# Kernel tuning notes

Hardware: AMD Instinct MI355X
Metric: run time of the kernel (lower is better)

## Reference

```python
import jax, jax.numpy as jnp
import numpy as np

B = 16384
IN = 512
H = 512

def setup_inputs() -> dict:
    key = jax.random.key(0)
    ks = jax.random.split(key, 8)
    inp = {
        "x_t": jax.random.normal(ks[0], (B, IN), dtype=jnp.float32),
        "h_t": jax.random.normal(ks[1], (B, H), dtype=jnp.float32),
        "W_ir": jax.random.normal(ks[2], (IN, H), dtype=jnp.float32),
        "W_hr": jax.random.normal(ks[3], (H, H), dtype=jnp.float32),
        "b_r": jnp.zeros((H,), dtype=jnp.float32),
        "W_iz": jax.random.normal(ks[4], (IN, H), dtype=jnp.float32),
        "W_hz": jax.random.normal(ks[5], (H, H), dtype=jnp.float32),
        "b_z": jnp.zeros((H,), dtype=jnp.float32),
        "W_in": jax.random.normal(ks[6], (IN, H), dtype=jnp.float32),
        "W_hn": jax.random.normal(ks[7], (H, H), dtype=jnp.float32),
        "b_n": jnp.zeros((H,), dtype=jnp.float32),
    }
    return inp

def reference(x_t, h_t, W_ir, W_hr, b_r, W_iz, W_hz, b_z, W_in, W_hn, b_n):
    # Fuse the three input-side and three hidden-side GEMMs by concatenating weights.
    Wi = jnp.concatenate([W_ir, W_iz, W_in], axis=1)   # [IN, 3H]
    Wh = jnp.concatenate([W_hr, W_hz, W_hn], axis=1)   # [H, 3H]
    gi = x_t @ Wi                                      # [B, 3H]
    gh = h_t @ Wh                                      # [B, 3H]
    h = b_r.shape[0]
    r_t = jax.nn.sigmoid(gi[:, :h] + gh[:, :h] + b_r)
    z_t = jax.nn.sigmoid(gi[:, h:2*h] + gh[:, h:2*h] + b_z)
    n_t = jnp.tanh(gi[:, 2*h:] + r_t * gh[:, 2*h:] + b_n)
    return (1.0 - z_t) * n_t + z_t * h_t
```

## Files before the change

kernel.cpp:

```cpp
#include <hip/hip_runtime.h>
#include <hip/hip_fp16.h>

typedef _Float16 half8 __attribute__((ext_vector_type(8)));
typedef float floatx4 __attribute__((ext_vector_type(4)));

#define AS1 __attribute__((address_space(1)))
#define AS3 __attribute__((address_space(3)))

#define WLO_OFF (6 * 512 * 512)
#define WMAT_STRIDE ((size_t)(8 * 16 * 2048))
#define APERM_OFF ((size_t)(2 * WLO_OFF))
#define APERM_HALFS ((size_t)128 * 16 * 4 * 4096)

__device__ __forceinline__ void async_lds16(const void* g, void* l) {
  __builtin_amdgcn_global_load_lds((const AS1 void*)g, (AS3 void*)l, 16, 0, 0);
}

__device__ __forceinline__ void permute_w_body(
    int b2, int t,
    const float* __restrict__ Wir, const float* __restrict__ Whr,
    const float* __restrict__ Wiz, const float* __restrict__ Whz,
    const float* __restrict__ Win, const float* __restrict__ Whn,
    _Float16* __restrict__ wperm, float* tile) {
  const int w = b2 >> 7;
  const int rem = b2 & 127;
  const int ki = rem >> 3;
  const int nt = rem & 7;
  const float* W = (w == 0) ? Wir : (w == 1) ? Whr : (w == 2) ? Wiz
                 : (w == 3) ? Whz : (w == 4) ? Win : Whn;
  const int k0 = ki * 32, n0 = nt * 64;
  const int kk = t >> 3;
  const int nn = (t & 7) * 8;
  const float* src = W + (k0 + kk) * 512 + n0 + nn;
  float4 f0 = *(const float4*)(src);
  float4 f1 = *(const float4*)(src + 4);
  float* drow = tile + kk * 68 + nn;
  *(float4*)(drow) = f0;
  *(float4*)(drow + 4) = f1;
  __syncthreads();
  const int u = t >> 6, l = t & 63;
  const int nloc = 16 * u + (l & 15);
  const int kbase = 8 * (l >> 4);
  half8 vh2, vl2;
#pragma unroll
  for (int j = 0; j < 8; ++j) {
    float f = tile[(kbase + j) * 68 + nloc];
    _Float16 hi = (_Float16)f;
    _Float16 lo = (_Float16)(f - (float)hi);
    vh2[j] = hi;
    vl2[j] = lo;
  }
  const size_t off = ((size_t)((w * 8 + nt) * 16 + ki)) * 2048 + t * 8;
  *(half8*)(wperm + off) = vh2;
  *(half8*)(wperm + WLO_OFF + off) = vl2;
}

__global__ __launch_bounds__(256) void prep(
    const float* __restrict__ x, const float* __restrict__ h,
    const float* __restrict__ Wir, const float* __restrict__ Whr,
    const float* __restrict__ Wiz, const float* __restrict__ Whz,
    const float* __restrict__ Win, const float* __restrict__ Whn,
    _Float16* __restrict__ wperm) {
  __shared__ __align__(16) float tile[32 * 68];
  const int b = blockIdx.x;
  const int t = threadIdx.x;

  if (b >= 2048) {
    permute_w_body(b - 2048, t, Wir, Whr, Wiz, Whz, Win, Whn, wperm, tile);
    return;
  }

  const int mt = b >> 4, kt = b & 15;
  _Float16* dst = wperm + APERM_OFF + ((size_t)(mt * 16 + kt)) * 16384;
  const int k0 = kt * 32;
#pragma unroll
  for (int hc = 0; hc < 2; ++hc) {
    const int c = t + hc * 256;
    const int m = 16 * (c >> 6) + (c & 15);
    const int kA = 8 * ((c >> 4) & 3);
    const float* px = x + ((size_t)(mt * 128 + m)) * 512 + k0 + kA;
    const float* ph = h + ((size_t)(mt * 128 + m)) * 512 + k0 + kA;
    float vx[8], vh[8];
    *(float4*)&vx[0] = *(const float4*)px;  *(float4*)&vx[4] = *(const float4*)(px + 4);
    *(float4*)&vh[0] = *(const float4*)ph;  *(float4*)&vh[4] = *(const float4*)(ph + 4);
    half8 xh, xl, hh, hl;
#pragma unroll
    for (int j = 0; j < 8; ++j) {
      _Float16 a = (_Float16)vx[j];
      xh[j] = a; xl[j] = (_Float16)(vx[j] - (float)a);
      _Float16 bb = (_Float16)vh[j];
      hh[j] = bb; hl[j] = (_Float16)(vh[j] - (float)bb);
    }
    *(half8*)(dst + 0 * 4096 + c * 8) = xh;
    *(half8*)(dst + 1 * 4096 + c * 8) = xl;
    *(half8*)(dst + 2 * 4096 + c * 8) = hh;
    *(half8*)(dst + 3 * 4096 + c * 8) = hl;
  }
}

__global__ __launch_bounds__(256) void permute_w(
    const float* __restrict__ Wir, const float* __restrict__ Whr,
    const float* __restrict__ Wiz, const float* __restrict__ Whz,
    const float* __restrict__ Win, const float* __restrict__ Whn,
    _Float16* __restrict__ wperm) {
  __shared__ __align__(16) float tile[32 * 68];
  permute_w_body(blockIdx.x, threadIdx.x, Wir, Whr, Wiz, Whz, Win, Whn, wperm, tile);
}

__global__ __launch_bounds__(256, 2) void gru_fused2(
    const float* __restrict__ h, const _Float16* __restrict__ wperm,
    const float* __restrict__ br, const float* __restrict__ bz,
    const float* __restrict__ bn, float* __restrict__ out) {
  __shared__ __align__(16) _Float16 ldsA[2 * 4 * 4096];

  const int t = threadIdx.x;
  const int lane = t & 63;
  const int wv = t >> 6;
  const int bid = blockIdx.x;
  const int xcd = bid & 7;
  const int g = bid >> 3;
  const int nt = g & 7;
  const int mt = (g >> 3) * 8 + xcd;
  const int m0 = mt * 128;
  const int n0 = nt * 64;
  const _Float16* wlo = wperm + WLO_OFF;
  const _Float16* aperm = wperm + APERM_OFF + (size_t)mt * 16 * 16384;

  floatx4 acc_r[8] = {};
  floatx4 acc_z[8] = {};
  floatx4 acc_in[8] = {};
  floatx4 acc_hn[8] = {};

  {
    const _Float16* asrc = aperm + wv * 4096 + lane * 8;
    _Float16* adst = ldsA + wv * 4096;
#pragma unroll
    for (int q = 0; q < 8; ++q) async_lds16(asrc + q * 512, adst + q * 512);
  }
  __syncthreads();

#pragma unroll 2
  for (int kt = 0; kt < 16; ++kt) {
    const _Float16* A = ldsA + (kt & 1) * 16384;

    const size_t tb = ((size_t)(nt * 16 + kt)) * 2048 + wv * 512 + lane * 8;
    half8 bh_ir = *(const half8*)(wperm + tb + 0 * WMAT_STRIDE);
    half8 bh_hr = *(const half8*)(wperm + tb + 1 * WMAT_STRIDE);
    half8 bh_iz = *(const half8*)(wperm + tb + 2 * WMAT_STRIDE);
    half8 bh_hz = *(const half8*)(wperm + tb + 3 * WMAT_STRIDE);
    half8 bh_in = *(const half8*)(wperm + tb + 4 * WMAT_STRIDE);
    half8 bh_hn = *(const half8*)(wperm + tb + 5 * WMAT_STRIDE);
    half8 bl_ir = *(const half8*)(wlo + tb + 0 * WMAT_STRIDE);
    half8 bl_hr = *(const half8*)(wlo + tb + 1 * WMAT_STRIDE);
    half8 bl_iz = *(const half8*)(wlo + tb + 2 * WMAT_STRIDE);
    half8 bl_hz = *(const half8*)(wlo + tb + 3 * WMAT_STRIDE);
    half8 bl_in = *(const half8*)(wlo + tb + 4 * WMAT_STRIDE);
    half8 bl_hn = *(const half8*)(wlo + tb + 5 * WMAT_STRIDE);
    __builtin_amdgcn_sched_barrier(0);

    if (kt < 15) {
      const _Float16* asrc =
          aperm + (size_t)(kt + 1) * 16384 + wv * 4096 + lane * 8;
      _Float16* adst = ldsA + ((kt & 1) ^ 1) * 16384 + wv * 4096;
#pragma unroll
      for (int q = 0; q < 8; ++q) async_lds16(asrc + q * 512, adst + q * 512);
    }
    __builtin_amdgcn_sched_barrier(0);

    __builtin_amdgcn_s_setprio(1);
#pragma unroll
    for (int i = 0; i < 8; ++i) {
      const int ao = (i * 64 + lane) * 8;
      half8 axh = *(const half8*)(A + 0 * 4096 + ao);
      half8 axl = *(const half8*)(A + 1 * 4096 + ao);
      half8 ahh = *(const half8*)(A + 2 * 4096 + ao);
      half8 ahl = *(const half8*)(A + 3 * 4096 + ao);
      acc_r[i]  = __builtin_amdgcn_mfma_f32_16x16x32_f16(axh, bh_ir, acc_r[i], 0, 0, 0);
      acc_r[i]  = __builtin_amdgcn_mfma_f32_16x16x32_f16(ahh, bh_hr, acc_r[i], 0, 0, 0);
      acc_z[i]  = __builtin_amdgcn_mfma_f32_16x16x32_f16(axh, bh_iz, acc_z[i], 0, 0, 0);
      acc_z[i]  = __builtin_amdgcn_mfma_f32_16x16x32_f16(ahh, bh_hz, acc_z[i], 0, 0, 0);
      acc_in[i] = __builtin_amdgcn_mfma_f32_16x16x32_f16(axh, bh_in, acc_in[i], 0, 0, 0);
      acc_hn[i] = __builtin_amdgcn_mfma_f32_16x16x32_f16(ahh, bh_hn, acc_hn[i], 0, 0, 0);
      acc_r[i]  = __builtin_amdgcn_mfma_f32_16x16x32_f16(axl, bh_ir, acc_r[i], 0, 0, 0);
      acc_r[i]  = __builtin_amdgcn_mfma_f32_16x16x32_f16(ahl, bh_hr, acc_r[i], 0, 0, 0);
      acc_z[i]  = __builtin_amdgcn_mfma_f32_16x16x32_f16(axl, bh_iz, acc_z[i], 0, 0, 0);
      acc_z[i]  = __builtin_amdgcn_mfma_f32_16x16x32_f16(ahl, bh_hz, acc_z[i], 0, 0, 0);
      acc_in[i] = __builtin_amdgcn_mfma_f32_16x16x32_f16(axl, bh_in, acc_in[i], 0, 0, 0);
      acc_hn[i] = __builtin_amdgcn_mfma_f32_16x16x32_f16(ahl, bh_hn, acc_hn[i], 0, 0, 0);
      acc_r[i]  = __builtin_amdgcn_mfma_f32_16x16x32_f16(axh, bl_ir, acc_r[i], 0, 0, 0);
      acc_r[i]  = __builtin_amdgcn_mfma_f32_16x16x32_f16(ahh, bl_hr, acc_r[i], 0, 0, 0);
      acc_z[i]  = __builtin_amdgcn_mfma_f32_16x16x32_f16(axh, bl_iz, acc_z[i], 0, 0, 0);
      acc_z[i]  = __builtin_amdgcn_mfma_f32_16x16x32_f16(ahh, bl_hz, acc_z[i], 0, 0, 0);
      acc_in[i] = __builtin_amdgcn_mfma_f32_16x16x32_f16(axh, bl_in, acc_in[i], 0, 0, 0);
      acc_hn[i] = __builtin_amdgcn_mfma_f32_16x16x32_f16(ahh, bl_hn, acc_hn[i], 0, 0, 0);
    }
    __builtin_amdgcn_s_setprio(0);

    __syncthreads();
  }

  const int quad = lane >> 4;
  const int col = lane & 15;
  const int n = n0 + wv * 16 + col;
  const float vbr = br[n], vbz = bz[n], vbn = bn[n];
#pragma unroll
  for (int i = 0; i < 8; ++i) {
    const int mbase = m0 + i * 16 + quad * 4;
#pragma unroll
    for (int r = 0; r < 4; ++r) {
      const int m = mbase + r;
      const float gr = acc_r[i][r] + vbr;
      const float gz = acc_z[i][r] + vbz;
      const float rg = 1.0f / (1.0f + __expf(-gr));
      const float zg = 1.0f / (1.0f + __expf(-gz));
      const float gn = acc_in[i][r] + rg * acc_hn[i][r] + vbn;
      const float e2 = __expf(2.0f * gn);
      const float ntv = 1.0f - 2.0f / (e2 + 1.0f);
      const float hp = h[m * 512 + n];
      out[m * 512 + n] = (1.0f - zg) * ntv + zg * hp;
    }
  }
}

__global__ __launch_bounds__(256, 2) void gru_fused_fb(
    const float* __restrict__ x, const float* __restrict__ h,
    const _Float16* __restrict__ wperm,
    const float* __restrict__ br, const float* __restrict__ bz,
    const float* __restrict__ bn, float* __restrict__ out) {
  __shared__ __align__(16) _Float16 ldsA[2 * 4 * 4096];
  const int t = threadIdx.x;
  const int lane = t & 63;
  const int wn = t >> 6;
  const int bid = blockIdx.x;
  const int nt = bid & 7;
  const int mt = bid >> 3;
  const int m0 = mt * 128;
  const int n0 = nt * 64;
  const _Float16* wlo = wperm + WLO_OFF;

  floatx4 acc_r[8] = {};
  floatx4 acc_z[8] = {};
  floatx4 acc_in[8] = {};
  floatx4 acc_hn[8] = {};

  const int mA = 16 * (t >> 6) + (t & 15);
  const int kA = 8 * ((t >> 4) & 3);
  const float* px0 = x + (m0 + mA) * 512 + kA;
  const float* ph0 = h + (m0 + mA) * 512 + kA;
  const float* px1 = px0 + 64 * 512;
  const float* ph1 = ph0 + 64 * 512;
  const int c0 = t, c1 = t + 256;

  {
    float v[4][8];
    *(float4*)&v[0][0] = *(const float4*)(px0); *(float4*)&v[0][4] = *(const float4*)(px0 + 4);
    *(float4*)&v[1][0] = *(const float4*)(px1); *(float4*)&v[1][4] = *(const float4*)(px1 + 4);
    *(float4*)&v[2][0] = *(const float4*)(ph0); *(float4*)&v[2][4] = *(const float4*)(ph0 + 4);
    *(float4*)&v[3][0] = *(const float4*)(ph1); *(float4*)&v[3][4] = *(const float4*)(ph1 + 4);
#pragma unroll
    for (int g = 0; g < 4; ++g) {
      half8 hi, lo;
#pragma unroll
      for (int j = 0; j < 8; ++j) {
        _Float16 a = (_Float16)v[g][j];
        hi[j] = a;
        lo[j] = (_Float16)(v[g][j] - (float)a);
      }
      const int c = (g & 1) ? c1 : c0;
      const int part = (g >> 1) * 2;
      *(half8*)(ldsA + (part + 0) * 4096 + c * 8) = hi;
      *(half8*)(ldsA + (part + 1) * 4096 + c * 8) = lo;
    }
  }
  __syncthreads();

#pragma unroll 2
  for (int kt = 0; kt < 16; ++kt) {
    const _Float16* A = ldsA + (kt & 1) * 16384;
    const size_t tb = ((size_t)(nt * 16 + kt)) * 2048 + wn * 512 + lane * 8;
    half8 bh_ir = *(const half8*)(wperm + tb + 0 * WMAT_STRIDE);
    half8 bh_hr = *(const half8*)(wperm + tb + 1 * WMAT_STRIDE);
    half8 bh_iz = *(const half8*)(wperm + tb + 2 * WMAT_STRIDE);
    half8 bh_hz = *(const half8*)(wperm + tb + 3 * WMAT_STRIDE);
    half8 bh_in = *(const half8*)(wperm + tb + 4 * WMAT_STRIDE);
    half8 bh_hn = *(const half8*)(wperm + tb + 5 * WMAT_STRIDE);
    half8 bl_ir = *(const half8*)(wlo + tb + 0 * WMAT_STRIDE);
    half8 bl_hr = *(const half8*)(wlo + tb + 1 * WMAT_STRIDE);
    half8 bl_iz = *(const half8*)(wlo + tb + 2 * WMAT_STRIDE);
    half8 bl_hz = *(const half8*)(wlo + tb + 3 * WMAT_STRIDE);
    half8 bl_in = *(const half8*)(wlo + tb + 4 * WMAT_STRIDE);
    half8 bl_hn = *(const half8*)(wlo + tb + 5 * WMAT_STRIDE);
    __builtin_amdgcn_sched_barrier(0);

    float v[4][8];
    if (kt < 15) {
      const int k0 = (kt + 1) * 32;
      *(float4*)&v[0][0] = *(const float4*)(px0 + k0); *(float4*)&v[0][4] = *(const float4*)(px0 + k0 + 4);
      *(float4*)&v[1][0] = *(const float4*)(px1 + k0); *(float4*)&v[1][4] = *(const float4*)(px1 + k0 + 4);
      *(float4*)&v[2][0] = *(const float4*)(ph0 + k0); *(float4*)&v[2][4] = *(const float4*)(ph0 + k0 + 4);
      *(float4*)&v[3][0] = *(const float4*)(ph1 + k0); *(float4*)&v[3][4] = *(const float4*)(ph1 + k0 + 4);
    }
    __builtin_amdgcn_sched_barrier(0);

    __builtin_amdgcn_s_setprio(1);
#pragma unroll
    for (int i = 0; i < 8; ++i) {
      const int ao = (i * 64 + lane) * 8;
      half8 axh = *(const half8*)(A + 0 * 4096 + ao);
      half8 axl = *(const half8*)(A + 1 * 4096 + ao);
      half8 ahh = *(const half8*)(A + 2 * 4096 + ao);
      half8 ahl = *(const half8*)(A + 3 * 4096 + ao);
      acc_r[i]  = __builtin_amdgcn_mfma_f32_16x16x32_f16(axh, bh_ir, acc_r[i], 0, 0, 0);
      acc_r[i]  = __builtin_amdgcn_mfma_f32_16x16x32_f16(ahh, bh_hr, acc_r[i], 0, 0, 0);
      acc_z[i]  = __builtin_amdgcn_mfma_f32_16x16x32_f16(axh, bh_iz, acc_z[i], 0, 0, 0);
      acc_z[i]  = __builtin_amdgcn_mfma_f32_16x16x32_f16(ahh, bh_hz, acc_z[i], 0, 0, 0);
      acc_in[i] = __builtin_amdgcn_mfma_f32_16x16x32_f16(axh, bh_in, acc_in[i], 0, 0, 0);
      acc_hn[i] = __builtin_amdgcn_mfma_f32_16x16x32_f16(ahh, bh_hn, acc_hn[i], 0, 0, 0);
      acc_r[i]  = __builtin_amdgcn_mfma_f32_16x16x32_f16(axl, bh_ir, acc_r[i], 0, 0, 0);
      acc_r[i]  = __builtin_amdgcn_mfma_f32_16x16x32_f16(ahl, bh_hr, acc_r[i], 0, 0, 0);
      acc_z[i]  = __builtin_amdgcn_mfma_f32_16x16x32_f16(axl, bh_iz, acc_z[i], 0, 0, 0);
      acc_z[i]  = __builtin_amdgcn_mfma_f32_16x16x32_f16(ahl, bh_hz, acc_z[i], 0, 0, 0);
      acc_in[i] = __builtin_amdgcn_mfma_f32_16x16x32_f16(axl, bh_in, acc_in[i], 0, 0, 0);
      acc_hn[i] = __builtin_amdgcn_mfma_f32_16x16x32_f16(ahl, bh_hn, acc_hn[i], 0, 0, 0);
      acc_r[i]  = __builtin_amdgcn_mfma_f32_16x16x32_f16(axh, bl_ir, acc_r[i], 0, 0, 0);
      acc_r[i]  = __builtin_amdgcn_mfma_f32_16x16x32_f16(ahh, bl_hr, acc_r[i], 0, 0, 0);
      acc_z[i]  = __builtin_amdgcn_mfma_f32_16x16x32_f16(axh, bl_iz, acc_z[i], 0, 0, 0);
      acc_z[i]  = __builtin_amdgcn_mfma_f32_16x16x32_f16(ahh, bl_hz, acc_z[i], 0, 0, 0);
      acc_in[i] = __builtin_amdgcn_mfma_f32_16x16x32_f16(axh, bl_in, acc_in[i], 0, 0, 0);
      acc_hn[i] = __builtin_amdgcn_mfma_f32_16x16x32_f16(ahh, bl_hn, acc_hn[i], 0, 0, 0);
    }
    __builtin_amdgcn_s_setprio(0);

    if (kt < 15) {
      _Float16* base = ldsA + ((kt & 1) ^ 1) * 16384;
#pragma unroll
      for (int g = 0; g < 4; ++g) {
        half8 hi, lo;
#pragma unroll
        for (int j = 0; j < 8; ++j) {
          _Float16 a = (_Float16)v[g][j];
          hi[j] = a;
          lo[j] = (_Float16)(v[g][j] - (float)a);
        }
        const int c = (g & 1) ? c1 : c0;
        const int part = (g >> 1) * 2;
        *(half8*)(base + (part + 0) * 4096 + c * 8) = hi;
        *(half8*)(base + (part + 1) * 4096 + c * 8) = lo;
      }
    }
    __syncthreads();
  }

  const int quad = lane >> 4;
  const int col = lane & 15;
  const int n = n0 + wn * 16 + col;
  const float vbr = br[n], vbz = bz[n], vbn = bn[n];
#pragma unroll
  for (int i = 0; i < 8; ++i) {
    const int mbase = m0 + i * 16 + quad * 4;
#pragma unroll
    for (int r = 0; r < 4; ++r) {
      const int m = mbase + r;
      const float gr = acc_r[i][r] + vbr;
      const float gz = acc_z[i][r] + vbz;
      const float rg = 1.0f / (1.0f + __expf(-gr));
      const float zg = 1.0f / (1.0f + __expf(-gz));
      const float gn = acc_in[i][r] + rg * acc_hn[i][r] + vbn;
      const float e2 = __expf(2.0f * gn);
      const float ntv = 1.0f - 2.0f / (e2 + 1.0f);
      const float hp = h[m * 512 + n];
      out[m * 512 + n] = (1.0f - zg) * ntv + zg * hp;
    }
  }
}

extern "C" void kernel_launch(void* const* d_in, const int* in_sizes, int n_in,
                              void* d_out, int out_size, void* d_ws, size_t ws_size,
                              hipStream_t stream) {
  const float* x   = (const float*)d_in[0];
  const float* h   = (const float*)d_in[1];
  const float* Wir = (const float*)d_in[2];
  const float* Whr = (const float*)d_in[3];
  const float* br  = (const float*)d_in[4];
  const float* Wiz = (const float*)d_in[5];
  const float* Whz = (const float*)d_in[6];
  const float* bz  = (const float*)d_in[7];
  const float* Win = (const float*)d_in[8];
  const float* Whn = (const float*)d_in[9];
  const float* bn  = (const float*)d_in[10];
  float* out = (float*)d_out;
  _Float16* wperm = (_Float16*)d_ws;

  const size_t need_bytes = (APERM_OFF + APERM_HALFS) * 2;
  if (ws_size >= need_bytes) {
    prep<<<2816, 256, 0, stream>>>(x, h, Wir, Whr, Wiz, Whz, Win, Whn, wperm);
    gru_fused2<<<1024, 256, 0, stream>>>(h, wperm, br, bz, bn, out);
  } else {
    permute_w<<<768, 256, 0, stream>>>(Wir, Whr, Wiz, Whz, Win, Whn, wperm);
    gru_fused_fb<<<1024, 256, 0, stream>>>(x, h, wperm, br, bz, bn, out);
  }
}
```

Before: 263.2 us.

## Interleave weight layout, software-pipeline B loads, and coalesce A prep via LDS

The weight buffer is re-laid out so that all twelve hi/lo fragments for one (n-tile, k-tile) sit next to each other. The main loop is split into two phases. The hi-weight MFMAs run while the lo weights load, and the next k-step's hi weights are prefetched into alternating register sets while the lo-weight MFMAs run. Manual vmcnt waits and raw barriers replace __syncthreads so that outstanding prefetches are not drained. The prep kernel now stages x and h through LDS so its global reads are coalesced row reads, at the cost of more registers and fragile hand-written wait counts.

```diff
diff --git a/kernel.cpp b/kernel.cpp
--- a/kernel.cpp
+++ b/kernel.cpp
@@ -7,23 +7,255 @@
 #define AS1 __attribute__((address_space(1)))
 #define AS3 __attribute__((address_space(3)))
 
+#define WTOT ((size_t)(8 * 16 * 12 * 2048))
+#define APERM_OFF WTOT
+#define APERM_HALFS ((size_t)128 * 16 * 4 * 4096)
 #define WLO_OFF (6 * 512 * 512)
 #define WMAT_STRIDE ((size_t)(8 * 16 * 2048))
-#define APERM_OFF ((size_t)(2 * WLO_OFF))
-#define APERM_HALFS ((size_t)128 * 16 * 4 * 4096)
 
 __device__ __forceinline__ void async_lds16(const void* g, void* l) {
   __builtin_amdgcn_global_load_lds((const AS1 void*)g, (AS3 void*)l, 16, 0, 0);
 }
 
-__device__ __forceinline__ void permute_w_body(
-    int b2, int t,
+__global__ __launch_bounds__(256) void prep(
+    const float* __restrict__ x, const float* __restrict__ h,
     const float* __restrict__ Wir, const float* __restrict__ Whr,
     const float* __restrict__ Wiz, const float* __restrict__ Whz,
     const float* __restrict__ Win, const float* __restrict__ Whn,
-    _Float16* __restrict__ wperm, float* tile) {
-  const int w = b2 >> 7;
-  const int rem = b2 & 127;
+    _Float16* __restrict__ wperm) {
+  __shared__ __align__(16) float xt[128 * 36];
+  __shared__ __align__(16) float ht[128 * 36];
+  const int b = blockIdx.x;
+  const int t = threadIdx.x;
+
+  if (b >= 2048) {
+    const int b2 = b - 2048;
+    const int w = b2 >> 7;
+    const int rem = b2 & 127;
+    const int ki = rem >> 3;
+    const int nt = rem & 7;
+    const float* W = (w == 0) ? Wir : (w == 1) ? Whr : (w == 2) ? Wiz
+                   : (w == 3) ? Whz : (w == 4) ? Win : Whn;
+    const int k0 = ki * 32, n0 = nt * 64;
+    const int kk = t >> 3;
+    const int nn = (t & 7) * 8;
+    const float* src = W + (k0 + kk) * 512 + n0 + nn;
+    float4 f0 = *(const float4*)(src);
+    float4 f1 = *(const float4*)(src + 4);
+    float* drow = xt + kk * 68 + nn;
+    *(float4*)(drow) = f0;
+    *(float4*)(drow + 4) = f1;
+    __syncthreads();
+    const int u = t >> 6, l = t & 63;
+    const int nloc = 16 * u + (l & 15);
+    const int kbase = 8 * (l >> 4);
+    half8 vh2, vl2;
+#pragma unroll
+    for (int j = 0; j < 8; ++j) {
+      float f = xt[(kbase + j) * 68 + nloc];
+      _Float16 hi = (_Float16)f;
+      _Float16 lo = (_Float16)(f - (float)hi);
+      vh2[j] = hi;
+      vl2[j] = lo;
+    }
+    const size_t base = ((size_t)((nt * 16 + ki) * 12)) * 2048 + t * 8;
+    *(half8*)(wperm + base + (size_t)w * 2048) = vh2;
+    *(half8*)(wperm + base + (size_t)(6 + w) * 2048) = vl2;
+    return;
+  }
+
+  const int mt = b >> 4, kt = b & 15;
+  const float* xb = x + ((size_t)(mt * 128)) * 512 + kt * 32;
+  const float* hb = h + ((size_t)(mt * 128)) * 512 + kt * 32;
+#pragma unroll
+  for (int p = 0; p < 2; ++p) {
+    const int r = (t >> 2) + p * 64;
+    const int c = (t & 3) * 8;
+    const float* sx = xb + (size_t)r * 512 + c;
+    const float* sh = hb + (size_t)r * 512 + c;
+    float4 a0 = *(const float4*)(sx);
+    float4 a1 = *(const float4*)(sx + 4);
+    float4 b0 = *(const float4*)(sh);
+    float4 b1 = *(const float4*)(sh + 4);
+    *(float4*)(xt + r * 36 + c) = a0;
+    *(float4*)(xt + r * 36 + c + 4) = a1;
+    *(float4*)(ht + r * 36 + c) = b0;
+    *(float4*)(ht + r * 36 + c + 4) = b1;
+  }
+  __syncthreads();
+  _Float16* dst = wperm + APERM_OFF + ((size_t)(mt * 16 + kt)) * 16384;
+#pragma unroll
+  for (int hc = 0; hc < 2; ++hc) {
+    const int cc = t + hc * 256;
+    const int m = 16 * (cc >> 6) + (cc & 15);
+    const int kA = 8 * ((cc >> 4) & 3);
+    half8 xh, xl, hh, hl;
+#pragma unroll
+    for (int j = 0; j < 8; ++j) {
+      float fx = xt[m * 36 + kA + j];
+      float fh = ht[m * 36 + kA + j];
+      _Float16 a = (_Float16)fx;
+      xh[j] = a; xl[j] = (_Float16)(fx - (float)a);
+      _Float16 bb = (_Float16)fh;
+      hh[j] = bb; hl[j] = (_Float16)(fh - (float)bb);
+    }
+    *(half8*)(dst + 0 * 4096 + cc * 8) = xh;
+    *(half8*)(dst + 1 * 4096 + cc * 8) = xl;
+    *(half8*)(dst + 2 * 4096 + cc * 8) = hh;
+    *(half8*)(dst + 3 * 4096 + cc * 8) = hl;
+  }
+}
+
+__global__ __launch_bounds__(256, 2) void gru_fused2(
+    const float* __restrict__ h, const _Float16* __restrict__ wperm,
+    const float* __restrict__ br, const float* __restrict__ bz,
+    const float* __restrict__ bn, float* __restrict__ out) {
+  __shared__ __align__(16) _Float16 ldsA[2 * 4 * 4096];
+
+  const int t = threadIdx.x;
+  const int lane = t & 63;
+  const int wv = t >> 6;
+  const int bid = blockIdx.x;
+  const int xcd = bid & 7;
+  const int g = bid >> 3;
+  const int nt = g & 7;
+  const int mt = (g >> 3) * 8 + xcd;
+  const int m0 = mt * 128;
+  const int n0 = nt * 64;
+  const _Float16* aperm = wperm + APERM_OFF + (size_t)mt * 16 * 16384;
+  const size_t wvoff = (size_t)wv * 512 + lane * 8;
+
+  floatx4 acc_r[8] = {};
+  floatx4 acc_z[8] = {};
+  floatx4 acc_in[8] = {};
+  floatx4 acc_hn[8] = {};
+
+  half8 bhA[6], bhB[6];
+
+  {
+    const _Float16* asrc = aperm + wv * 4096 + lane * 8;
+    _Float16* adst = ldsA + wv * 4096;
+#pragma unroll
+    for (int q = 0; q < 8; ++q) async_lds16(asrc + q * 512, adst + q * 512);
+    const _Float16* wb = wperm + ((size_t)(nt * 16 + 0) * 12) * 2048 + wvoff;
+#pragma unroll
+    for (int m = 0; m < 6; ++m) bhA[m] = *(const half8*)(wb + (size_t)m * 2048);
+  }
+  asm volatile("s_waitcnt vmcnt(6)" ::: "memory");
+  __builtin_amdgcn_s_barrier();
+  __builtin_amdgcn_sched_barrier(0);
+
+#define GRU_STEP(KT, BH, BHN)                                                  \
+  do {                                                                         \
+    const int kt_ = (KT);                                                      \
+    const _Float16* A = ldsA + (kt_ & 1) * 16384;                              \
+    const _Float16* wb =                                                       \
+        wperm + ((size_t)(nt * 16 + kt_) * 12) * 2048 + wvoff;                 \
+    half8 bl[6];                                                               \
+    _Pragma("unroll")                                                          \
+    for (int m = 0; m < 6; ++m)                                                \
+      bl[m] = *(const half8*)(wb + (size_t)(6 + m) * 2048);                    \
+    __builtin_amdgcn_sched_barrier(0);                                         \
+    if (kt_ < 15) {                                                            \
+      const _Float16* asrc =                                                   \
+          aperm + (size_t)(kt_ + 1) * 16384 + wv * 4096 + lane * 8;            \
+      _Float16* adst = ldsA + ((kt_ & 1) ^ 1) * 16384 + wv * 4096;             \
+      _Pragma("unroll")                                                        \
+      for (int q = 0; q < 8; ++q)                                              \
+        async_lds16(asrc + q * 512, adst + q * 512);                           \
+    }                                                                          \
+    __builtin_amdgcn_sched_barrier(0);                                         \
+    __builtin_amdgcn_s_setprio(1);                                             \
+    _Pragma("unroll")                                                          \
+    for (int i = 0; i < 8; ++i) {                                              \
+      const int ao = (i * 64 + lane) * 8;                                      \
+      half8 axh = *(const half8*)(A + 0 * 4096 + ao);                          \
+      half8 axl = *(const half8*)(A + 1 * 4096 + ao);                          \
+      half8 ahh = *(const half8*)(A + 2 * 4096 + ao);                          \
+      half8 ahl = *(const half8*)(A + 3 * 4096 + ao);                          \
+      acc_r[i]  = __builtin_amdgcn_mfma_f32_16x16x32_f16(axh, BH[0], acc_r[i], 0, 0, 0);  \
+      acc_z[i]  = __builtin_amdgcn_mfma_f32_16x16x32_f16(axh, BH[2], acc_z[i], 0, 0, 0);  \
+      acc_in[i] = __builtin_amdgcn_mfma_f32_16x16x32_f16(axh, BH[4], acc_in[i], 0, 0, 0); \
+      acc_hn[i] = __builtin_amdgcn_mfma_f32_16x16x32_f16(ahh, BH[5], acc_hn[i], 0, 0, 0); \
+      acc_r[i]  = __builtin_amdgcn_mfma_f32_16x16x32_f16(ahh, BH[1], acc_r[i], 0, 0, 0);  \
+      acc_z[i]  = __builtin_amdgcn_mfma_f32_16x16x32_f16(ahh, BH[3], acc_z[i], 0, 0, 0);  \
+      acc_in[i] = __builtin_amdgcn_mfma_f32_16x16x32_f16(axl, BH[4], acc_in[i], 0, 0, 0); \
+      acc_hn[i] = __builtin_amdgcn_mfma_f32_16x16x32_f16(ahl, BH[5], acc_hn[i], 0, 0, 0); \
+      acc_r[i]  = __builtin_amdgcn_mfma_f32_16x16x32_f16(axl, BH[0], acc_r[i], 0, 0, 0);  \
+      acc_z[i]  = __builtin_amdgcn_mfma_f32_16x16x32_f16(axl, BH[2], acc_z[i], 0, 0, 0);  \
+      acc_r[i]  = __builtin_amdgcn_mfma_f32_16x16x32_f16(ahl, BH[1], acc_r[i], 0, 0, 0);  \
+      acc_z[i]  = __builtin_amdgcn_mfma_f32_16x16x32_f16(ahl, BH[3], acc_z[i], 0, 0, 0);  \
+    }                                                                          \
+    __builtin_amdgcn_s_setprio(0);                                             \
+    __builtin_amdgcn_sched_barrier(0);                                         \
+    if (kt_ < 15) {                                                            \
+      const _Float16* wbn =                                                    \
+          wperm + ((size_t)(nt * 16 + kt_ + 1) * 12) * 2048 + wvoff;           \
+      _Pragma("unroll")                                                        \
+      for (int m = 0; m < 6; ++m)                                              \
+        BHN[m] = *(const half8*)(wbn + (size_t)m * 2048);                      \
+    }                                                                          \
+    __builtin_amdgcn_sched_barrier(0);                                         \
+    __builtin_amdgcn_s_setprio(1);                                             \
+    _Pragma("unroll")                                                          \
+    for (int i = 0; i < 8; ++i) {                                              \
+      const int ao = (i * 64 + lane) * 8;                                      \
+      half8 axh = *(const half8*)(A + 0 * 4096 + ao);                          \
+      half8 ahh = *(const half8*)(A + 2 * 4096 + ao);                          \
+      acc_r[i]  = __builtin_amdgcn_mfma_f32_16x16x32_f16(axh, bl[0], acc_r[i], 0, 0, 0);  \
+      acc_z[i]  = __builtin_amdgcn_mfma_f32_16x16x32_f16(axh, bl[2], acc_z[i], 0, 0, 0);  \
+      acc_in[i] = __builtin_amdgcn_mfma_f32_16x16x32_f16(axh, bl[4], acc_in[i], 0, 0, 0); \
+      acc_hn[i] = __builtin_amdgcn_mfma_f32_16x16x32_f16(ahh, bl[5], acc_hn[i], 0, 0, 0); \
+      acc_r[i]  = __builtin_amdgcn_mfma_f32_16x16x32_f16(ahh, bl[1], acc_r[i], 0, 0, 0);  \
+      acc_z[i]  = __builtin_amdgcn_mfma_f32_16x16x32_f16(ahh, bl[3], acc_z[i], 0, 0, 0);  \
+    }                                                                          \
+    __builtin_amdgcn_s_setprio(0);                                             \
+    if (kt_ < 15) {                                                            \
+      asm volatile("s_waitcnt vmcnt(6)" ::: "memory");                         \
+      __builtin_amdgcn_s_barrier();                                            \
+      __builtin_amdgcn_sched_barrier(0);                                       \
+    }                                                                          \
+  } while (0)
+
+  for (int kt2 = 0; kt2 < 16; kt2 += 2) {
+    GRU_STEP(kt2, bhA, bhB);
+    GRU_STEP(kt2 + 1, bhB, bhA);
+  }
+#undef GRU_STEP
+
+  const int quad = lane >> 4;
+  const int col = lane & 15;
+  const int n = n0 + wv * 16 + col;
+  const float vbr = br[n], vbz = bz[n], vbn = bn[n];
+#pragma unroll
+  for (int i = 0; i < 8; ++i) {
+    const int mbase = m0 + i * 16 + quad * 4;
+#pragma unroll
+    for (int r = 0; r < 4; ++r) {
+      const int m = mbase + r;
+      const float gr = acc_r[i][r] + vbr;
+      const float gz = acc_z[i][r] + vbz;
+      const float rg = 1.0f / (1.0f + __expf(-gr));
+      const float zg = 1.0f / (1.0f + __expf(-gz));
+      const float gn = acc_in[i][r] + rg * acc_hn[i][r] + vbn;
+      const float e2 = __expf(2.0f * gn);
+      const float ntv = 1.0f - 2.0f / (e2 + 1.0f);
+      const float hp = h[m * 512 + n];
+      out[m * 512 + n] = (1.0f - zg) * ntv + zg * hp;
+    }
+  }
+}
+
+__global__ __launch_bounds__(256) void permute_w_old(
+    const float* __restrict__ Wir, const float* __restrict__ Whr,
+    const float* __restrict__ Wiz, const float* __restrict__ Whz,
+    const float* __restrict__ Win, const float* __restrict__ Whn,
+    _Float16* __restrict__ wperm) {
+  __shared__ __align__(16) float tile[32 * 68];
+  const int b = blockIdx.x;
+  const int t = threadIdx.x;
+  const int w = b >> 7;
+  const int rem = b & 127;
   const int ki = rem >> 3;
   const int nt = rem & 7;
   const float* W = (w == 0) ? Wir : (w == 1) ? Whr : (w == 2) ? Wiz
@@ -55,95 +287,62 @@
   *(half8*)(wperm + WLO_OFF + off) = vl2;
 }
 
-__global__ __launch_bounds__(256) void prep(
+__global__ __launch_bounds__(256, 2) void gru_fused_fb(
     const float* __restrict__ x, const float* __restrict__ h,
-    const float* __restrict__ Wir, const float* __restrict__ Whr,
-    const float* __restrict__ Wiz, const float* __restrict__ Whz,
-    const float* __restrict__ Win, const float* __restrict__ Whn,
-    _Float16* __restrict__ wperm) {
-  __shared__ __align__(16) float tile[32 * 68];
-  const int b = blockIdx.x;
-  const int t = threadIdx.x;
-
-  if (b >= 2048) {
-    permute_w_body(b - 2048, t, Wir, Whr, Wiz, Whz, Win, Whn, wperm, tile);
-    return;
-  }
-
-  const int mt = b >> 4, kt = b & 15;
-  _Float16* dst = wperm + APERM_OFF + ((size_t)(mt * 16 + kt)) * 16384;
-  const int k0 = kt * 32;
-#pragma unroll
-  for (int hc = 0; hc < 2; ++hc) {
-    const int c = t + hc * 256;
-    const int m = 16 * (c >> 6) + (c & 15);
-    const int kA = 8 * ((c >> 4) & 3);
-    const float* px = x + ((size_t)(mt * 128 + m)) * 512 + k0 + kA;
-    const float* ph = h + ((size_t)(mt * 128 + m)) * 512 + k0 + kA;
-    float vx[8], vh[8];
-    *(float4*)&vx[0] = *(const float4*)px;  *(float4*)&vx[4] = *(const float4*)(px + 4);
-    *(float4*)&vh[0] = *(const float4*)ph;  *(float4*)&vh[4] = *(const float4*)(ph + 4);
-    half8 xh, xl, hh, hl;
-#pragma unroll
-    for (int j = 0; j < 8; ++j) {
-      _Float16 a = (_Float16)vx[j];
-      xh[j] = a; xl[j] = (_Float16)(vx[j] - (float)a);
-      _Float16 bb = (_Float16)vh[j];
-      hh[j] = bb; hl[j] = (_Float16)(vh[j] - (float)bb);
-    }
-    *(half8*)(dst + 0 * 4096 + c * 8) = xh;
-    *(half8*)(dst + 1 * 4096 + c * 8) = xl;
-    *(half8*)(dst + 2 * 4096 + c * 8) = hh;
-    *(half8*)(dst + 3 * 4096 + c * 8) = hl;
-  }
-}
-
-__global__ __launch_bounds__(256) void permute_w(
-    const float* __restrict__ Wir, const float* __restrict__ Whr,
-    const float* __restrict__ Wiz, const float* __restrict__ Whz,
-    const float* __restrict__ Win, const float* __restrict__ Whn,
-    _Float16* __restrict__ wperm) {
-  __shared__ __align__(16) float tile[32 * 68];
-  permute_w_body(blockIdx.x, threadIdx.x, Wir, Whr, Wiz, Whz, Win, Whn, wperm, tile);
-}
-
-__global__ __launch_bounds__(256, 2) void gru_fused2(
-    const float* __restrict__ h, const _Float16* __restrict__ wperm,
+    const _Float16* __restrict__ wperm,
     const float* __restrict__ br, const float* __restrict__ bz,
     const float* __restrict__ bn, float* __restrict__ out) {
   __shared__ __align__(16) _Float16 ldsA[2 * 4 * 4096];
-
   const int t = threadIdx.x;
   const int lane = t & 63;
-  const int wv = t >> 6;
+  const int wn = t >> 6;
   const int bid = blockIdx.x;
-  const int xcd = bid & 7;
-  const int g = bid >> 3;
-  const int nt = g & 7;
-  const int mt = (g >> 3) * 8 + xcd;
+  const int nt = bid & 7;
+  const int mt = bid >> 3;
   const int m0 = mt * 128;
   const int n0 = nt * 64;
   const _Float16* wlo = wperm + WLO_OFF;
-  const _Float16* aperm = wperm + APERM_OFF + (size_t)mt * 16 * 16384;
 
   floatx4 acc_r[8] = {};
   floatx4 acc_z[8] = {};
   floatx4 acc_in[8] = {};
   floatx4 acc_hn[8] = {};
 
+  const int mA = 16 * (t >> 6) + (t & 15);
+  const int kA = 8 * ((t >> 4) & 3);
+  const float* px0 = x + (m0 + mA) * 512 + kA;
+  const float* ph0 = h + (m0 + mA) * 512 + kA;
+  const float* px1 = px0 + 64 * 512;
+  const float* ph1 = ph0 + 64 * 512;
+  const int c0 = t, c1 = t + 256;
+
   {
-    const _Float16* asrc = aperm + wv * 4096 + lane * 8;
-    _Float16* adst = ldsA + wv * 4096;
-#pragma unroll
-    for (int q = 0; q < 8; ++q) async_lds16(asrc + q * 512, adst + q * 512);
+    float v[4][8];
+    *(float4*)&v[0][0] = *(const float4*)(px0); *(float4*)&v[0][4] = *(const float4*)(px0 + 4);
+    *(float4*)&v[1][0] = *(const float4*)(px1); *(float4*)&v[1][4] = *(const float4*)(px1 + 4);
+    *(float4*)&v[2][0] = *(const float4*)(ph0); *(float4*)&v[2][4] = *(const float4*)(ph0 + 4);
+    *(float4*)&v[3][0] = *(const float4*)(ph1); *(float4*)&v[3][4] = *(const float4*)(ph1 + 4);
+#pragma unroll
+    for (int g = 0; g < 4; ++g) {
+      half8 hi, lo;
+#pragma unroll
+      for (int j = 0; j < 8; ++j) {
+        _Float16 a = (_Float16)v[g][j];
+        hi[j] = a;
+        lo[j] = (_Float16)(v[g][j] - (float)a);
+      }
+      const int c = (g & 1) ? c1 : c0;
+      const int part = (g >> 1) * 2;
+      *(half8*)(ldsA + (part + 0) * 4096 + c * 8) = hi;
+      *(half8*)(ldsA + (part + 1) * 4096 + c * 8) = lo;
+    }
   }
   __syncthreads();
 
 #pragma unroll 2
   for (int kt = 0; kt < 16; ++kt) {
     const _Float16* A = ldsA + (kt & 1) * 16384;
-
-    const size_t tb = ((size_t)(nt * 16 + kt)) * 2048 + wv * 512 + lane * 8;
+    const size_t tb = ((size_t)(nt * 16 + kt)) * 2048 + wn * 512 + lane * 8;
     half8 bh_ir = *(const half8*)(wperm + tb + 0 * WMAT_STRIDE);
     half8 bh_hr = *(const half8*)(wperm + tb + 1 * WMAT_STRIDE);
     half8 bh_iz = *(const half8*)(wperm + tb + 2 * WMAT_STRIDE);
@@ -158,12 +357,13 @@
     half8 bl_hn = *(const half8*)(wlo + tb + 5 * WMAT_STRIDE);
     __builtin_amdgcn_sched_barrier(0);
 
+    float v[4][8];
     if (kt < 15) {
-      const _Float16* asrc =
-          aperm + (size_t)(kt + 1) * 16384 + wv * 4096 + lane * 8;
-      _Float16* adst = ldsA + ((kt & 1) ^ 1) * 16384 + wv * 4096;
-#pragma unroll
-      for (int q = 0; q < 8; ++q) async_lds16(asrc + q * 512, adst + q * 512);
+      const int k0 = (kt + 1) * 32;
+      *(float4*)&v[0][0] = *(const float4*)(px0 + k0); *(float4*)&v[0][4] = *(const float4*)(px0 + k0 + 4);
+      *(float4*)&v[1][0] = *(const float4*)(px1 + k0); *(float4*)&v[1][4] = *(const float4*)(px1 + k0 + 4);
+      *(float4*)&v[2][0] = *(const float4*)(ph0 + k0); *(float4*)&v[2][4] = *(const float4*)(ph0 + k0 + 4);
+      *(float4*)&v[3][0] = *(const float4*)(ph1 + k0); *(float4*)&v[3][4] = *(const float4*)(ph1 + k0 + 4);
     }
     __builtin_amdgcn_sched_barrier(0);
 
@@ -196,141 +396,6 @@
     }
     __builtin_amdgcn_s_setprio(0);
 
-    __syncthreads();
-  }
-
-  const int quad = lane >> 4;
-  const int col = lane & 15;
-  const int n = n0 + wv * 16 + col;
-  const float vbr = br[n], vbz = bz[n], vbn = bn[n];
-#pragma unroll
-  for (int i = 0; i < 8; ++i) {
-    const int mbase = m0 + i * 16 + quad * 4;
-#pragma unroll
-    for (int r = 0; r < 4; ++r) {
-      const int m = mbase + r;
-      const float gr = acc_r[i][r] + vbr;
-      const float gz = acc_z[i][r] + vbz;
-      const float rg = 1.0f / (1.0f + __expf(-gr));
-      const float zg = 1.0f / (1.0f + __expf(-gz));
-      const float gn = acc_in[i][r] + rg * acc_hn[i][r] + vbn;
-      const float e2 = __expf(2.0f * gn);
-      const float ntv = 1.0f - 2.0f / (e2 + 1.0f);
-      const float hp = h[m * 512 + n];
-      out[m * 512 + n] = (1.0f - zg) * ntv + zg * hp;
-    }
-  }
-}
-
-__global__ __launch_bounds__(256, 2) void gru_fused_fb(
-    const float* __restrict__ x, const float* __restrict__ h,
-    const _Float16* __restrict__ wperm,
-    const float* __restrict__ br, const float* __restrict__ bz,
-    const float* __restrict__ bn, float* __restrict__ out) {
-  __shared__ __align__(16) _Float16 ldsA[2 * 4 * 4096];
-  const int t = threadIdx.x;
-  const int lane = t & 63;
-  const int wn = t >> 6;
-  const int bid = blockIdx.x;
-  const int nt = bid & 7;
-  const int mt = bid >> 3;
-  const int m0 = mt * 128;
-  const int n0 = nt * 64;
-  const _Float16* wlo = wperm + WLO_OFF;
-
-  floatx4 acc_r[8] = {};
-  floatx4 acc_z[8] = {};
-  floatx4 acc_in[8] = {};
-  floatx4 acc_hn[8] = {};
-
-  const int mA = 16 * (t >> 6) + (t & 15);
-  const int kA = 8 * ((t >> 4) & 3);
-  const float* px0 = x + (m0 + mA) * 512 + kA;
-  const float* ph0 = h + (m0 + mA) * 512 + kA;
-  const float* px1 = px0 + 64 * 512;
-  const float* ph1 = ph0 + 64 * 512;
-  const int c0 = t, c1 = t + 256;
-
-  {
-    float v[4][8];
-    *(float4*)&v[0][0] = *(const float4*)(px0); *(float4*)&v[0][4] = *(const float4*)(px0 + 4);
-    *(float4*)&v[1][0] = *(const float4*)(px1); *(float4*)&v[1][4] = *(const float4*)(px1 + 4);
-    *(float4*)&v[2][0] = *(const float4*)(ph0); *(float4*)&v[2][4] = *(const float4*)(ph0 + 4);
-    *(float4*)&v[3][0] = *(const float4*)(ph1); *(float4*)&v[3][4] = *(const float4*)(ph1 + 4);
-#pragma unroll
-    for (int g = 0; g < 4; ++g) {
-      half8 hi, lo;
-#pragma unroll
-      for (int j = 0; j < 8; ++j) {
-        _Float16 a = (_Float16)v[g][j];
-        hi[j] = a;
-        lo[j] = (_Float16)(v[g][j] - (float)a);
-      }
-      const int c = (g & 1) ? c1 : c0;
-      const int part = (g >> 1) * 2;
-      *(half8*)(ldsA + (part + 0) * 4096 + c * 8) = hi;
-      *(half8*)(ldsA + (part + 1) * 4096 + c * 8) = lo;
-    }
-  }
-  __syncthreads();
-
-#pragma unroll 2
-  for (int kt = 0; kt < 16; ++kt) {
-    const _Float16* A = ldsA + (kt & 1) * 16384;
-    const size_t tb = ((size_t)(nt * 16 + kt)) * 2048 + wn * 512 + lane * 8;
-    half8 bh_ir = *(const half8*)(wperm + tb + 0 * WMAT_STRIDE);
-    half8 bh_hr = *(const half8*)(wperm + tb + 1 * WMAT_STRIDE);
-    half8 bh_iz = *(const half8*)(wperm + tb + 2 * WMAT_STRIDE);
-    half8 bh_hz = *(const half8*)(wperm + tb + 3 * WMAT_STRIDE);
-    half8 bh_in = *(const half8*)(wperm + tb + 4 * WMAT_STRIDE);
-    half8 bh_hn = *(const half8*)(wperm + tb + 5 * WMAT_STRIDE);
-    half8 bl_ir = *(const half8*)(wlo + tb + 0 * WMAT_STRIDE);
-    half8 bl_hr = *(const half8*)(wlo + tb + 1 * WMAT_STRIDE);
-    half8 bl_iz = *(const half8*)(wlo + tb + 2 * WMAT_STRIDE);
-    half8 bl_hz = *(const half8*)(wlo + tb + 3 * WMAT_STRIDE);
-    half8 bl_in = *(const half8*)(wlo + tb + 4 * WMAT_STRIDE);
-    half8 bl_hn = *(const half8*)(wlo + tb + 5 * WMAT_STRIDE);
-    __builtin_amdgcn_sched_barrier(0);
-
-    float v[4][8];
-    if (kt < 15) {
-      const int k0 = (kt + 1) * 32;
-      *(float4*)&v[0][0] = *(const float4*)(px0 + k0); *(float4*)&v[0][4] = *(const float4*)(px0 + k0 + 4);
-      *(float4*)&v[1][0] = *(const float4*)(px1 + k0); *(float4*)&v[1][4] = *(const float4*)(px1 + k0 + 4);
-      *(float4*)&v[2][0] = *(const float4*)(ph0 + k0); *(float4*)&v[2][4] = *(const float4*)(ph0 + k0 + 4);
-      *(float4*)&v[3][0] = *(const float4*)(ph1 + k0); *(float4*)&v[3][4] = *(const float4*)(ph1 + k0 + 4);
-    }
-    __builtin_amdgcn_sched_barrier(0);
-
-    __builtin_amdgcn_s_setprio(1);
-#pragma unroll
-    for (int i = 0; i < 8; ++i) {
-      const int ao = (i * 64 + lane) * 8;
-      half8 axh = *(const half8*)(A + 0 * 4096 + ao);
-      half8 axl = *(const half8*)(A + 1 * 4096 + ao);
-      half8 ahh = *(const half8*)(A + 2 * 4096 + ao);
-      half8 ahl = *(const half8*)(A + 3 * 4096 + ao);
-      acc_r[i]  = __builtin_amdgcn_mfma_f32_16x16x32_f16(axh, bh_ir, acc_r[i], 0, 0, 0);
-      acc_r[i]  = __builtin_amdgcn_mfma_f32_16x16x32_f16(ahh, bh_hr, acc_r[i], 0, 0, 0);
-      acc_z[i]  = __builtin_amdgcn_mfma_f32_16x16x32_f16(axh, bh_iz, acc_z[i], 0, 0, 0);
-      acc_z[i]  = __builtin_amdgcn_mfma_f32_16x16x32_f16(ahh, bh_hz, acc_z[i], 0, 0, 0);
-      acc_in[i] = __builtin_amdgcn_mfma_f32_16x16x32_f16(axh, bh_in, acc_in[i], 0, 0, 0);
-      acc_hn[i] = __builtin_amdgcn_mfma_f32_16x16x32_f16(ahh, bh_hn, acc_hn[i], 0, 0, 0);
-      acc_r[i]  = __builtin_amdgcn_mfma_f32_16x16x32_f16(axl, bh_ir, acc_r[i], 0, 0, 0);
-      acc_r[i]  = __builtin_amdgcn_mfma_f32_16x16x32_f16(ahl, bh_hr, acc_r[i], 0, 0, 0);
-      acc_z[i]  = __builtin_amdgcn_mfma_f32_16x16x32_f16(axl, bh_iz, acc_z[i], 0, 0, 0);
-      acc_z[i]  = __builtin_amdgcn_mfma_f32_16x16x32_f16(ahl, bh_hz, acc_z[i], 0, 0, 0);
-      acc_in[i] = __builtin_amdgcn_mfma_f32_16x16x32_f16(axl, bh_in, acc_in[i], 0, 0, 0);
-      acc_hn[i] = __builtin_amdgcn_mfma_f32_16x16x32_f16(ahl, bh_hn, acc_hn[i], 0, 0, 0);
-      acc_r[i]  = __builtin_amdgcn_mfma_f32_16x16x32_f16(axh, bl_ir, acc_r[i], 0, 0, 0);
-      acc_r[i]  = __builtin_amdgcn_mfma_f32_16x16x32_f16(ahh, bl_hr, acc_r[i], 0, 0, 0);
-      acc_z[i]  = __builtin_amdgcn_mfma_f32_16x16x32_f16(axh, bl_iz, acc_z[i], 0, 0, 0);
-      acc_z[i]  = __builtin_amdgcn_mfma_f32_16x16x32_f16(ahh, bl_hz, acc_z[i], 0, 0, 0);
-      acc_in[i] = __builtin_amdgcn_mfma_f32_16x16x32_f16(axh, bl_in, acc_in[i], 0, 0, 0);
-      acc_hn[i] = __builtin_amdgcn_mfma_f32_16x16x32_f16(ahh, bl_hn, acc_hn[i], 0, 0, 0);
-    }
-    __builtin_amdgcn_s_setprio(0);
-
     if (kt < 15) {
       _Float16* base = ldsA + ((kt & 1) ^ 1) * 16384;
 #pragma unroll
@@ -396,7 +461,7 @@
     prep<<<2816, 256, 0, stream>>>(x, h, Wir, Whr, Wiz, Whz, Win, Whn, wperm);
     gru_fused2<<<1024, 256, 0, stream>>>(h, wperm, br, bz, bn, out);
   } else {
-    permute_w<<<768, 256, 0, stream>>>(Wir, Whr, Wiz, Whz, Win, Whn, wperm);
+    permute_w_old<<<768, 256, 0, stream>>>(Wir, Whr, Wiz, Whz, Win, Whn, wperm);
     gru_fused_fb<<<1024, 256, 0, stream>>>(x, h, wperm, br, bz, bn, out);
   }
 }
```

New measurement: 280.7 us. 1.07x slower.
